# Performance work log

Hardware: AMD Instinct MI355X
Metric: run time of the kernel (lower is better)

## Reference

```python
import jax, jax.numpy as jnp
import numpy as np

N_INST = 50000
D_IN, D_HID, D_ATT = 1024, 512, 256  # size_dict['small']
N_ENS = 4
N_CLS = 2
CB_SIZE = 256
BETA = 0.25
TOP_K = 1


def setup_inputs() -> dict:
    key = jax.random.key(0)
    ks = jax.random.split(key, 9)
    h = jax.random.normal(ks[0], (N_INST, D_IN), dtype=jnp.float32)
    fc_W = jax.random.normal(ks[1], (D_IN, D_HID), dtype=jnp.float32) * (1.0 / np.sqrt(D_IN))
    fc_b = jnp.zeros((D_HID,), dtype=jnp.float32)
    Ua = jax.random.normal(ks[2], (N_ENS, D_HID, D_ATT), dtype=jnp.float32) * (1.0 / np.sqrt(D_HID))
    Ub = jax.random.normal(ks[3], (N_ENS, D_HID, D_ATT), dtype=jnp.float32) * (1.0 / np.sqrt(D_HID))
    Uc = jax.random.normal(ks[4], (N_ENS, D_ATT, 1), dtype=jnp.float32) * (1.0 / np.sqrt(D_ATT))
    cls_W = jax.random.normal(ks[5], (D_HID, N_CLS), dtype=jnp.float32) * (1.0 / np.sqrt(D_HID))
    cls_b = jnp.zeros((N_CLS,), dtype=jnp.float32)
    codebook = jax.random.normal(ks[6], (CB_SIZE, D_HID), dtype=jnp.float32)
    return {"h": h, "fc_W": fc_W, "fc_b": fc_b, "Ua": Ua, "Ub": Ub,
            "Uc": Uc, "cls_W": cls_W, "cls_b": cls_b, "codebook": codebook}


def _vector_quantization(M, codebook):
    # NOTE: original code uses +2*matmul (sign bug in torch source); kept faithful.
    dist = (jnp.sum(M * M, axis=1, keepdims=True)
            + jnp.sum(codebook * codebook, axis=1)
            + 2.0 * (M @ codebook.T))                      # [1, CB]
    inds = jnp.argmin(dist, axis=1)                        # [1]
    one_hot = jax.nn.one_hot(inds, CB_SIZE, dtype=M.dtype)  # [1, CB]
    q = one_hot @ codebook                                  # [1, D_HID]
    commitment = jnp.mean((jax.lax.stop_gradient(q) - M) ** 2)
    embedding = jnp.mean((q - jax.lax.stop_gradient(M)) ** 2)
    vq_loss = commitment * BETA + embedding
    q_st = M + jax.lax.stop_gradient(q - M)  # straight-through (unused downstream)
    return vq_loss, q_st


def reference(h, fc_W, fc_b, Ua, Ub, Uc, cls_W, cls_b, codebook):
    # fc + ReLU: [n, D_HID]
    x = jax.nn.relu(h @ fc_W + fc_b)
    # gated batch-ensemble attention (ensemble dim n=4 broadcast)
    xe = jnp.broadcast_to(x[None], (N_ENS, x.shape[0], D_HID))
    a = jnp.tanh(jnp.einsum('ndk,nkl->ndl', xe, Ua))         # [4, n, D_ATT]
    b = jax.nn.sigmoid(jnp.einsum('ndk,nkl->ndl', xe, Ub))   # [4, n, D_ATT]
    A = jnp.einsum('ndk,nkl->ndl', a * b, Uc).sum(0)          # [n, 1]
    A = jax.nn.sigmoid(A.T)                                   # [1, n]
    M = (A @ x) / jnp.sum(A)                                  # [1, D_HID]
    vq_loss, _M_code = _vector_quantization(M, codebook)
    logits = M @ cls_W + cls_b                                # [1, N_CLS]
    y_probs = jax.nn.softmax(logits, axis=1)
    _, top_idx = jax.lax.top_k(y_probs[:, 1], TOP_K)          # [1]
    top_instance = logits[top_idx]                            # [1, N_CLS]
    Y_hat = jnp.argmax(top_instance, axis=1)[:, None]         # [1, 1] int
    Y_prob = jax.nn.softmax(top_instance, axis=1)
    return (top_instance, Y_prob, Y_hat, vq_loss, y_probs, A)
```

## Files before the change

kernel.cpp:

```cpp
#include <hip/hip_runtime.h>
#include <hip/hip_bf16.h>
#include <math.h>

typedef __bf16 bf16_t;
typedef __bf16 bf16x8 __attribute__((ext_vector_type(8)));
typedef float  f32x4  __attribute__((ext_vector_type(4)));

#define MINST 50000

typedef const __attribute__((address_space(1))) void* gas1_t;
typedef __attribute__((address_space(3))) void* las3_t;
__device__ __forceinline__ void gload16(const void* g, const void* l){
  __builtin_amdgcn_global_load_lds((gas1_t)g, (las3_t)l, 16, 0, 0);
}

__device__ __forceinline__ float fast_sigmoid(float x){
  return __fdividef(1.f, 1.f + __expf(-x));
}
__device__ __forceinline__ float fast_tanh(float x){
  float e = __expf(2.f*x);
  return 1.f - __fdividef(2.f, e + 1.f);
}

__global__ void prep_wt(const float* __restrict__ W, bf16_t* __restrict__ WT){
  int idx = blockIdx.x*256 + threadIdx.x;
  if (idx >= 512*1024) return;
  int n = idx >> 10, k = idx & 1023;
  WT[idx] = (bf16_t)W[k*512 + n];
}

__global__ void prep_uab(const float* __restrict__ Ua, const float* __restrict__ Ub,
                         bf16_t* __restrict__ UabT){
  int idx = blockIdx.x*256 + threadIdx.x;
  if (idx >= 2048*512) return;
  int c = idx >> 9, k = idx & 511;
  int s = c & 1, t = c >> 1;
  int n = t >> 8, l = t & 255;
  const float* src = s ? Ub : Ua;
  UabT[idx] = (bf16_t)src[(n*512 + k)*256 + l];
}

__global__ void zero_ws_k(float* __restrict__ Alogit, float* __restrict__ Mbuf){
  int i = blockIdx.x*256 + threadIdx.x;
  if (i < MINST) Alogit[i] = 0.f;
  if (i < 513)   Mbuf[i]  = 0.f;
}

template<int EPI, int K, int NBY>
__global__ __launch_bounds__(256, 2)
void gemm_k(const void* __restrict__ Ap, const bf16_t* __restrict__ Bp, int M,
            const float* __restrict__ bias, bf16_t* __restrict__ Xout,
            const float* __restrict__ Uc, float* __restrict__ Alogit)
{
  __shared__ bf16_t As[(EPI==0?1:2)][128*32] __attribute__((aligned(16)));
  __shared__ bf16_t Bs[2][128*32] __attribute__((aligned(16)));

  const int tid  = threadIdx.x;
  const int lane = tid & 63;
  const int w    = tid >> 6;
  const int wr   = w >> 1;
  const int wc   = w & 1;

  const int nwg = gridDim.x;
  const int q = nwg >> 3, r = nwg & 7;
  const int x = blockIdx.x & 7, pos = blockIdx.x >> 3;
  const int logical = (x < r ? x*(q+1) : r*(q+1) + (x-r)*q) + pos;
  const int m0 = (logical / NBY) * 128;
  const int n0 = (logical % NBY) * 128;

  const f32x4 fzero = {0.f, 0.f, 0.f, 0.f};
  f32x4 acc[4][4];
#pragma unroll
  for (int m = 0; m < 4; ++m)
#pragma unroll
    for (int n = 0; n < 4; ++n) acc[m][n] = fzero;

  const int srow = lane >> 2;
  const int schk = (lane & 3) * 8;
  const bf16_t* bsrc0 = Bp + (size_t)(n0 + w*32 + srow)*K + schk;
  const bf16_t* bsrc1 = bsrc0 + (size_t)16*K;

  auto stageB = [&](int buf, int k0){
    gload16(bsrc0 + k0, &Bs[buf][(w*32     )*32]);
    gload16(bsrc1 + k0, &Bs[buf][(w*32 + 16)*32]);
  };

  const bf16_t* asrc0 = (const bf16_t*)Ap + (size_t)(m0 + w*32 + srow)*K + schk;
  const bf16_t* asrc1 = asrc0 + (size_t)16*K;
  auto stageA1 = [&](int buf, int k0){
    gload16(asrc0 + k0, &As[buf][(w*32     )*32]);
    gload16(asrc1 + k0, &As[buf][(w*32 + 16)*32]);
  };

  const int a_row  = tid >> 1;
  const int a_half = tid & 1;
  f32x4 sAf[4];
  auto loadA0 = [&](int k0){
    const float* A = (const float*)Ap;
    int gr = m0 + a_row;
    if (gr < M) {
      const f32x4* p = (const f32x4*)(A + (size_t)gr*K + k0 + a_half*16);
      sAf[0]=p[0]; sAf[1]=p[1]; sAf[2]=p[2]; sAf[3]=p[3];
    } else {
      sAf[0]=fzero; sAf[1]=fzero; sAf[2]=fzero; sAf[3]=fzero;
    }
  };
  auto writeA0 = [&](){
    bf16x8 lo, hi;
#pragma unroll
    for (int j = 0; j < 4; ++j) {
      lo[j]   = (bf16_t)sAf[0][j];
      lo[4+j] = (bf16_t)sAf[1][j];
      hi[j]   = (bf16_t)sAf[2][j];
      hi[4+j] = (bf16_t)sAf[3][j];
    }
    *(bf16x8*)&As[0][a_row*32 + a_half*16    ] = lo;
    *(bf16x8*)&As[0][a_row*32 + a_half*16 + 8] = hi;
  };

  const int fr = lane & 15;
  const int kh = lane >> 4;
  constexpr int NT = K / 32;

  if constexpr (EPI == 0) {
    loadA0(0);
    stageB(0, 0);
#pragma unroll 4
    for (int kt = 0; kt < NT; ++kt) {
      const int cur = kt & 1;
      __syncthreads();
      writeA0();
      __syncthreads();
      if (kt + 1 < NT) { loadA0((kt+1)*32); stageB(cur^1, (kt+1)*32); }
      bf16x8 a[4], b[4];
#pragma unroll
      for (int m = 0; m < 4; ++m)
        a[m] = *(const bf16x8*)&As[0][(wr*64 + m*16 + fr)*32 + kh*8];
#pragma unroll
      for (int n = 0; n < 4; ++n)
        b[n] = *(const bf16x8*)&Bs[cur][(wc*64 + n*16 + fr)*32 + kh*8];
#pragma unroll
      for (int m = 0; m < 4; ++m)
#pragma unroll
        for (int n = 0; n < 4; ++n)
          acc[m][n] = __builtin_amdgcn_mfma_f32_16x16x32_bf16(a[m], b[n], acc[m][n], 0, 0, 0);
    }
  } else {
    stageA1(0, 0);
    stageB(0, 0);
#pragma unroll 4
    for (int kt = 0; kt < NT; ++kt) {
      const int cur = kt & 1;
      __syncthreads();
      if (kt + 1 < NT) { stageA1(cur^1, (kt+1)*32); stageB(cur^1, (kt+1)*32); }
      bf16x8 a[4], b[4];
#pragma unroll
      for (int m = 0; m < 4; ++m)
        a[m] = *(const bf16x8*)&As[cur][(wr*64 + m*16 + fr)*32 + kh*8];
#pragma unroll
      for (int n = 0; n < 4; ++n)
        b[n] = *(const bf16x8*)&Bs[cur][(wc*64 + n*16 + fr)*32 + kh*8];
#pragma unroll
      for (int m = 0; m < 4; ++m)
#pragma unroll
        for (int n = 0; n < 4; ++n)
          acc[m][n] = __builtin_amdgcn_mfma_f32_16x16x32_bf16(a[m], b[n], acc[m][n], 0, 0, 0);
    }
  }

  const int rg = lane >> 4;
  if constexpr (EPI == 0) {
#pragma unroll
    for (int n = 0; n < 4; ++n) {
      int col = n0 + wc*64 + n*16 + fr;
      float bv = bias[col];
#pragma unroll
      for (int m = 0; m < 4; ++m)
#pragma unroll
        for (int rr = 0; rr < 4; ++rr) {
          int row = m0 + wr*64 + m*16 + rg*4 + rr;
          if (row < M) {
            float v = acc[m][n][rr] + bv;
            Xout[(size_t)row*512 + col] = (bf16_t)(v > 0.f ? v : 0.f);
          }
        }
    }
  } else {
    float gacc[4][4];
#pragma unroll
    for (int m = 0; m < 4; ++m)
#pragma unroll
      for (int rr = 0; rr < 4; ++rr) gacc[m][rr] = 0.f;
    const bool even = (lane & 1) == 0;
#pragma unroll
    for (int n = 0; n < 4; ++n) {
      int col = n0 + wc*64 + n*16 + fr;
      float ucv = Uc[col >> 1];
#pragma unroll
      for (int m = 0; m < 4; ++m)
#pragma unroll
        for (int rr = 0; rr < 4; ++rr) {
          float v = acc[m][n][rr];
          float tv = even ? fast_tanh(v) : fast_sigmoid(v);
          float pv = __shfl_xor(tv, 1);
          gacc[m][rr] += tv * pv * ucv;
        }
    }
#pragma unroll
    for (int m = 0; m < 4; ++m)
#pragma unroll
      for (int rr = 0; rr < 4; ++rr) {
        float s = gacc[m][rr];
        s += __shfl_xor(s, 1);
        s += __shfl_xor(s, 2);
        s += __shfl_xor(s, 4);
        s += __shfl_xor(s, 8);
        if (fr == 0) {
          int row = m0 + wr*64 + m*16 + rg*4 + rr;
          if (row < M) atomicAdd(&Alogit[row], 0.5f * s);
        }
      }
  }
}

__global__ void a_final(const float* __restrict__ Alogit, float* __restrict__ outA,
                        float* __restrict__ sumA){
  int i = blockIdx.x*256 + threadIdx.x;
  float a = 0.f;
  if (i < MINST) { a = fast_sigmoid(Alogit[i]); outA[i] = a; }
  float s = a;
#pragma unroll
  for (int o = 1; o < 64; o <<= 1) s += __shfl_xor(s, o);
  __shared__ float wsum[4];
  int lane = threadIdx.x & 63, w = threadIdx.x >> 6;
  if (lane == 0) wsum[w] = s;
  __syncthreads();
  if (threadIdx.x == 0) atomicAdd(sumA, wsum[0]+wsum[1]+wsum[2]+wsum[3]);
}

__global__ void m_reduce(const bf16_t* __restrict__ Xb, const float* __restrict__ Aout,
                         float* __restrict__ Mbuf){
  int t = threadIdx.x;
  int c0 = (t & 63) * 8;
  float acc[8];
#pragma unroll
  for (int j = 0; j < 8; ++j) acc[j] = 0.f;
  for (int r = blockIdx.x*4 + (t>>6); r < MINST; r += gridDim.x*4) {
    float a = Aout[r];
    bf16x8 xv = *(const bf16x8*)(Xb + (size_t)r*512 + c0);
#pragma unroll
    for (int j = 0; j < 8; ++j) acc[j] += a * (float)xv[j];
  }
#pragma unroll
  for (int j = 0; j < 8; ++j) atomicAdd(&Mbuf[c0 + j], acc[j]);
}

__device__ __forceinline__ float block_sum256(float v, float* red){
  int t = threadIdx.x;
  red[t] = v; __syncthreads();
  for (int s = 128; s > 0; s >>= 1) {
    if (t < s) red[t] += red[t+s];
    __syncthreads();
  }
  float rr = red[0];
  __syncthreads();
  return rr;
}

__global__ __launch_bounds__(256)
void finalize_k(const float* __restrict__ Mbuf, const float* __restrict__ cb,
                const float* __restrict__ clsW, const float* __restrict__ clsb,
                float* __restrict__ dout)
{
  __shared__ float Mn[512];
  __shared__ float red[256];
  __shared__ float dist[256];
  __shared__ int   idxs[256];
  __shared__ int   indS;
  int t = threadIdx.x;
  float sA = Mbuf[512];
  Mn[t]     = Mbuf[t]     / sA;
  Mn[t+256] = Mbuf[t+256] / sA;
  __syncthreads();
  float msq_p = Mn[t]*Mn[t] + Mn[t+256]*Mn[t+256];
  float Msq = block_sum256(msq_p, red);

  const float* cbr = cb + t*512;
  float cs = 0.f, dt = 0.f;
  for (int k = 0; k < 512; k += 4) {
    f32x4 c = *(const f32x4*)(cbr + k);
    cs += c[0]*c[0] + c[1]*c[1] + c[2]*c[2] + c[3]*c[3];
    dt += Mn[k]*c[0] + Mn[k+1]*c[1] + Mn[k+2]*c[2] + Mn[k+3]*c[3];
  }
  dist[t] = Msq + cs + 2.f*dt;
  idxs[t] = t;
  __syncthreads();
  for (int s = 128; s > 0; s >>= 1) {
    if (t < s && dist[t+s] < dist[t]) { dist[t] = dist[t+s]; idxs[t] = idxs[t+s]; }
    __syncthreads();
  }
  if (t == 0) indS = idxs[0];
  __syncthreads();

  const float* qv = cb + (size_t)indS*512;
  float d0 = qv[t]     - Mn[t];
  float d1 = qv[t+256] - Mn[t+256];
  float vqs = block_sum256(d0*d0 + d1*d1, red);
  float vq_loss = 1.25f * (vqs / 512.f);

  float p0 = Mn[t]*clsW[t*2]   + Mn[t+256]*clsW[(t+256)*2];
  float p1 = Mn[t]*clsW[t*2+1] + Mn[t+256]*clsW[(t+256)*2+1];
  float l0 = block_sum256(p0, red);
  float l1 = block_sum256(p1, red);

  if (t == 0) {
    l0 += clsb[0]; l1 += clsb[1];
    float mx = fmaxf(l0, l1);
    float e0 = __expf(l0 - mx), e1 = __expf(l1 - mx);
    float si = e0 + e1;
    float y0 = e0 / si, y1 = e1 / si;
    int yhat = (l1 > l0) ? 1 : 0;
    dout[0] = l0; dout[1] = l1;
    dout[2] = y0; dout[3] = y1;
    dout[4] = (float)yhat;
    dout[5] = vq_loss;
    dout[6] = y0; dout[7] = y1;
  }
}

extern "C" void kernel_launch(void* const* d_in, const int* in_sizes, int n_in,
                              void* d_out, int out_size, void* d_ws, size_t ws_size,
                              hipStream_t stream) {
  const float* h    = (const float*)d_in[0];
  const float* fcW  = (const float*)d_in[1];
  const float* fcb  = (const float*)d_in[2];
  const float* Ua   = (const float*)d_in[3];
  const float* Ub   = (const float*)d_in[4];
  const float* Uc   = (const float*)d_in[5];
  const float* clsW = (const float*)d_in[6];
  const float* clsb = (const float*)d_in[7];
  const float* cbk  = (const float*)d_in[8];
  float* out = (float*)d_out;

  char* ws = (char*)d_ws;
  bf16_t* Xb     = (bf16_t*)ws;
  bf16_t* WT     = (bf16_t*)(ws + 51200000);
  bf16_t* UabT   = (bf16_t*)(ws + 52248576);
  float*  Alogit = (float*)(ws + 54345728);
  float*  Mbuf   = (float*)(ws + 54545728);

  const int M = MINST;

  prep_wt <<<2048, 256, 0, stream>>>(fcW, WT);
  prep_uab<<<4096, 256, 0, stream>>>(Ua, Ub, UabT);
  zero_ws_k<<<196, 256, 0, stream>>>(Alogit, Mbuf);

  gemm_k<0,1024,4><<<1564, 256, 0, stream>>>(h, WT, M, fcb, Xb, nullptr, nullptr);
  gemm_k<1, 512,16><<<6256, 256, 0, stream>>>(Xb, UabT, M, nullptr, nullptr, Uc, Alogit);

  a_final <<<196, 256, 0, stream>>>(Alogit, out + 8, Mbuf + 512);
  m_reduce<<<128, 256, 0, stream>>>(Xb, out + 8, Mbuf);
  finalize_k<<<1, 256, 0, stream>>>(Mbuf, cbk, clsW, clsb, out);
}
```

Measured before the change: 507.1 us.

## Split GEMM kernels, add multi-chunk triple-buffered attention GEMM with swizzled LDS

The templated GEMM is split in two. The fc GEMM now stages B through registers into padded (stride-40) LDS instead of direct global-to-LDS loads, and uses a plain 2D grid without the XCD remap. The attention GEMM now has each workgroup loop over four 128-column chunks, reusing one A row-tile across 512 output columns. It uses a triple-buffered LDS pipeline with explicit vmcnt waits, an XOR swizzle to avoid bank conflicts, and s_setprio around the MFMAs. The goal is fewer redundant Xb reads, fewer atomics and fewer launches, at the cost of longer-running workgroups; m_reduce also gets twice as many blocks.

```diff
diff --git a/kernel.cpp b/kernel.cpp
--- a/kernel.cpp
+++ b/kernel.cpp
@@ -4,6 +4,7 @@
 
 typedef __bf16 bf16_t;
 typedef __bf16 bf16x8 __attribute__((ext_vector_type(8)));
+typedef __bf16 bf16x2 __attribute__((ext_vector_type(2)));
 typedef float  f32x4  __attribute__((ext_vector_type(4)));
 
 #define MINST 50000
@@ -46,27 +47,20 @@
   if (i < 513)   Mbuf[i]  = 0.f;
 }
 
-template<int EPI, int K, int NBY>
 __global__ __launch_bounds__(256, 2)
-void gemm_k(const void* __restrict__ Ap, const bf16_t* __restrict__ Bp, int M,
-            const float* __restrict__ bias, bf16_t* __restrict__ Xout,
-            const float* __restrict__ Uc, float* __restrict__ Alogit)
+void gemm_fc(const float* __restrict__ Ap, const bf16_t* __restrict__ Bp, int M,
+             const float* __restrict__ bias, bf16_t* __restrict__ Xout)
 {
-  __shared__ bf16_t As[(EPI==0?1:2)][128*32] __attribute__((aligned(16)));
-  __shared__ bf16_t Bs[2][128*32] __attribute__((aligned(16)));
-
+  constexpr int K = 1024;
+  __shared__ bf16_t As[128*40] __attribute__((aligned(16)));
+  __shared__ bf16_t Bs[128*40] __attribute__((aligned(16)));
   const int tid  = threadIdx.x;
   const int lane = tid & 63;
-  const int w    = tid >> 6;
-  const int wr   = w >> 1;
-  const int wc   = w & 1;
-
-  const int nwg = gridDim.x;
-  const int q = nwg >> 3, r = nwg & 7;
-  const int x = blockIdx.x & 7, pos = blockIdx.x >> 3;
-  const int logical = (x < r ? x*(q+1) : r*(q+1) + (x-r)*q) + pos;
-  const int m0 = (logical / NBY) * 128;
-  const int n0 = (logical % NBY) * 128;
+  const int wid  = tid >> 6;
+  const int wr   = wid >> 1;
+  const int wc   = wid & 1;
+  const int m0   = blockIdx.x * 128;
+  const int n0   = blockIdx.y * 128;
 
   const f32x4 fzero = {0.f, 0.f, 0.f, 0.f};
   f32x4 acc[4][4];
@@ -75,37 +69,29 @@
 #pragma unroll
     for (int n = 0; n < 4; ++n) acc[m][n] = fzero;
 
-  const int srow = lane >> 2;
-  const int schk = (lane & 3) * 8;
-  const bf16_t* bsrc0 = Bp + (size_t)(n0 + w*32 + srow)*K + schk;
-  const bf16_t* bsrc1 = bsrc0 + (size_t)16*K;
-
-  auto stageB = [&](int buf, int k0){
-    gload16(bsrc0 + k0, &Bs[buf][(w*32     )*32]);
-    gload16(bsrc1 + k0, &Bs[buf][(w*32 + 16)*32]);
-  };
-
-  const bf16_t* asrc0 = (const bf16_t*)Ap + (size_t)(m0 + w*32 + srow)*K + schk;
-  const bf16_t* asrc1 = asrc0 + (size_t)16*K;
-  auto stageA1 = [&](int buf, int k0){
-    gload16(asrc0 + k0, &As[buf][(w*32     )*32]);
-    gload16(asrc1 + k0, &As[buf][(w*32 + 16)*32]);
-  };
-
+  const int q_row  = tid >> 2;
+  const int q_c    = tid & 3;
   const int a_row  = tid >> 1;
   const int a_half = tid & 1;
-  f32x4 sAf[4];
-  auto loadA0 = [&](int k0){
-    const float* A = (const float*)Ap;
+
+  bf16x8 sB0, sB1;
+  f32x4  sAf[4];
+
+  auto loadTiles = [&](int k0){
+    sB0 = *(const bf16x8*)(Bp + (size_t)(n0 + q_row     )*K + k0 + q_c*8);
+    sB1 = *(const bf16x8*)(Bp + (size_t)(n0 + q_row + 64)*K + k0 + q_c*8);
     int gr = m0 + a_row;
     if (gr < M) {
-      const f32x4* p = (const f32x4*)(A + (size_t)gr*K + k0 + a_half*16);
+      const f32x4* p = (const f32x4*)(Ap + (size_t)gr*K + k0 + a_half*16);
       sAf[0]=p[0]; sAf[1]=p[1]; sAf[2]=p[2]; sAf[3]=p[3];
     } else {
       sAf[0]=fzero; sAf[1]=fzero; sAf[2]=fzero; sAf[3]=fzero;
     }
   };
-  auto writeA0 = [&](){
+
+  auto storeTiles = [&](){
+    *(bf16x8*)&Bs[(q_row     )*40 + q_c*8] = sB0;
+    *(bf16x8*)&Bs[(q_row + 64)*40 + q_c*8] = sB1;
     bf16x8 lo, hi;
 #pragma unroll
     for (int j = 0; j < 4; ++j) {
@@ -114,113 +100,168 @@
       hi[j]   = (bf16_t)sAf[2][j];
       hi[4+j] = (bf16_t)sAf[3][j];
     }
-    *(bf16x8*)&As[0][a_row*32 + a_half*16    ] = lo;
-    *(bf16x8*)&As[0][a_row*32 + a_half*16 + 8] = hi;
+    *(bf16x8*)&As[a_row*40 + a_half*16    ] = lo;
+    *(bf16x8*)&As[a_row*40 + a_half*16 + 8] = hi;
   };
 
+  loadTiles(0);
   const int fr = lane & 15;
   const int kh = lane >> 4;
   constexpr int NT = K / 32;
-
-  if constexpr (EPI == 0) {
-    loadA0(0);
-    stageB(0, 0);
-#pragma unroll 4
-    for (int kt = 0; kt < NT; ++kt) {
-      const int cur = kt & 1;
-      __syncthreads();
-      writeA0();
-      __syncthreads();
-      if (kt + 1 < NT) { loadA0((kt+1)*32); stageB(cur^1, (kt+1)*32); }
-      bf16x8 a[4], b[4];
-#pragma unroll
-      for (int m = 0; m < 4; ++m)
-        a[m] = *(const bf16x8*)&As[0][(wr*64 + m*16 + fr)*32 + kh*8];
+  for (int kt = 0; kt < NT; ++kt) {
+    __syncthreads();
+    storeTiles();
+    __syncthreads();
+    if (kt + 1 < NT) loadTiles((kt+1)*32);
+    bf16x8 a[4], b[4];
+#pragma unroll
+    for (int m = 0; m < 4; ++m)
+      a[m] = *(const bf16x8*)&As[(wr*64 + m*16 + fr)*40 + kh*8];
+#pragma unroll
+    for (int n = 0; n < 4; ++n)
+      b[n] = *(const bf16x8*)&Bs[(wc*64 + n*16 + fr)*40 + kh*8];
+#pragma unroll
+    for (int m = 0; m < 4; ++m)
 #pragma unroll
       for (int n = 0; n < 4; ++n)
-        b[n] = *(const bf16x8*)&Bs[cur][(wc*64 + n*16 + fr)*32 + kh*8];
-#pragma unroll
-      for (int m = 0; m < 4; ++m)
-#pragma unroll
-        for (int n = 0; n < 4; ++n)
-          acc[m][n] = __builtin_amdgcn_mfma_f32_16x16x32_bf16(a[m], b[n], acc[m][n], 0, 0, 0);
-    }
-  } else {
-    stageA1(0, 0);
-    stageB(0, 0);
-#pragma unroll 4
-    for (int kt = 0; kt < NT; ++kt) {
-      const int cur = kt & 1;
-      __syncthreads();
-      if (kt + 1 < NT) { stageA1(cur^1, (kt+1)*32); stageB(cur^1, (kt+1)*32); }
-      bf16x8 a[4], b[4];
-#pragma unroll
-      for (int m = 0; m < 4; ++m)
-        a[m] = *(const bf16x8*)&As[cur][(wr*64 + m*16 + fr)*32 + kh*8];
-#pragma unroll
-      for (int n = 0; n < 4; ++n)
-        b[n] = *(const bf16x8*)&Bs[cur][(wc*64 + n*16 + fr)*32 + kh*8];
-#pragma unroll
-      for (int m = 0; m < 4; ++m)
-#pragma unroll
-        for (int n = 0; n < 4; ++n)
-          acc[m][n] = __builtin_amdgcn_mfma_f32_16x16x32_bf16(a[m], b[n], acc[m][n], 0, 0, 0);
-    }
+        acc[m][n] = __builtin_amdgcn_mfma_f32_16x16x32_bf16(a[m], b[n], acc[m][n], 0, 0, 0);
   }
 
   const int rg = lane >> 4;
-  if constexpr (EPI == 0) {
-#pragma unroll
-    for (int n = 0; n < 4; ++n) {
-      int col = n0 + wc*64 + n*16 + fr;
-      float bv = bias[col];
-#pragma unroll
-      for (int m = 0; m < 4; ++m)
-#pragma unroll
-        for (int rr = 0; rr < 4; ++rr) {
-          int row = m0 + wr*64 + m*16 + rg*4 + rr;
-          if (row < M) {
-            float v = acc[m][n][rr] + bv;
-            Xout[(size_t)row*512 + col] = (bf16_t)(v > 0.f ? v : 0.f);
-          }
-        }
-    }
-  } else {
-    float gacc[4][4];
+#pragma unroll
+  for (int n = 0; n < 4; ++n) {
+    int col = n0 + wc*64 + n*16 + fr;
+    float bv = bias[col];
 #pragma unroll
     for (int m = 0; m < 4; ++m)
 #pragma unroll
-      for (int rr = 0; rr < 4; ++rr) gacc[m][rr] = 0.f;
-    const bool even = (lane & 1) == 0;
-#pragma unroll
-    for (int n = 0; n < 4; ++n) {
-      int col = n0 + wc*64 + n*16 + fr;
-      float ucv = Uc[col >> 1];
-#pragma unroll
-      for (int m = 0; m < 4; ++m)
-#pragma unroll
-        for (int rr = 0; rr < 4; ++rr) {
-          float v = acc[m][n][rr];
-          float tv = even ? fast_tanh(v) : fast_sigmoid(v);
-          float pv = __shfl_xor(tv, 1);
-          gacc[m][rr] += tv * pv * ucv;
-        }
-    }
-#pragma unroll
-    for (int m = 0; m < 4; ++m)
-#pragma unroll
       for (int rr = 0; rr < 4; ++rr) {
-        float s = gacc[m][rr];
-        s += __shfl_xor(s, 1);
-        s += __shfl_xor(s, 2);
-        s += __shfl_xor(s, 4);
-        s += __shfl_xor(s, 8);
-        if (fr == 0) {
-          int row = m0 + wr*64 + m*16 + rg*4 + rr;
-          if (row < M) atomicAdd(&Alogit[row], 0.5f * s);
+        int row = m0 + wr*64 + m*16 + rg*4 + rr;
+        if (row < M) {
+          float v = acc[m][n][rr] + bv;
+          Xout[(size_t)row*512 + col] = (bf16_t)(v > 0.f ? v : 0.f);
         }
       }
   }
+}
+
+__global__ __launch_bounds__(256)
+void gemm_att(const bf16_t* __restrict__ Xb, const bf16_t* __restrict__ Bp, int M,
+              const float* __restrict__ Uc, float* __restrict__ Alogit)
+{
+  constexpr int K = 512, NCH = 4, NTC = 16, TOT = NCH*NTC;
+  __shared__ bf16_t As[3][128*32] __attribute__((aligned(16)));
+  __shared__ bf16_t Bs[3][128*32] __attribute__((aligned(16)));
+
+  const int tid  = threadIdx.x;
+  const int lane = tid & 63;
+  const int w    = tid >> 6;
+  const int wr   = w >> 1;
+  const int wc   = w & 1;
+
+  const int nwg = gridDim.x;
+  const int q = nwg >> 3, r = nwg & 7;
+  const int x = blockIdx.x & 7, pos = blockIdx.x >> 3;
+  const int logical = (x < r ? x*(q+1) : r*(q+1) + (x-r)*q) + pos;
+  const int m0 = (logical >> 2) * 128;
+  const int nb = (logical & 3) * 512;
+
+  const f32x4 fzero = {0.f, 0.f, 0.f, 0.f};
+  f32x4 acc[4][4];
+  float gacc[4][4];
+#pragma unroll
+  for (int m = 0; m < 4; ++m)
+#pragma unroll
+    for (int n = 0; n < 4; ++n){ acc[m][n] = fzero; gacc[m][n] = 0.f; }
+
+  const int sr  = lane >> 2;
+  const int scc = (lane & 3) ^ ((lane >> 3) & 3);
+  const bf16_t* aS0 = Xb + (size_t)(m0 + w*32 +      sr)*K + scc*8;
+  const bf16_t* aS1 = Xb + (size_t)(m0 + w*32 + 16 + sr)*K + scc*8;
+  const bf16_t* bS0 = Bp + (size_t)(nb + w*32 +      sr)*K + scc*8;
+  const bf16_t* bS1 = Bp + (size_t)(nb + w*32 + 16 + sr)*K + scc*8;
+
+  auto stage = [&](int it2, int buf){
+    const int c2  = it2 >> 4;
+    const int kt2 = it2 & 15;
+    const size_t boff = (size_t)c2*(128*K) + kt2*32;
+    gload16(aS0 + kt2*32, &As[buf][(w*32     )*32]);
+    gload16(aS1 + kt2*32, &As[buf][(w*32 + 16)*32]);
+    gload16(bS0 + boff,   &Bs[buf][(w*32     )*32]);
+    gload16(bS1 + boff,   &Bs[buf][(w*32 + 16)*32]);
+  };
+
+  const int fr = lane & 15;
+  const int kh = lane >> 4;
+  const int ca = (kh ^ ((fr >> 1) & 3)) * 8;
+  const bool even = (lane & 1) == 0;
+
+  stage(0, 0);
+  stage(1, 1);
+  int cur = 0, sb = 2;
+  for (int it = 0; it < TOT; ++it){
+    if (it + 1 < TOT) asm volatile("s_waitcnt vmcnt(4)" ::: "memory");
+    else              asm volatile("s_waitcnt vmcnt(0)" ::: "memory");
+    __builtin_amdgcn_s_barrier();
+    if (it + 2 < TOT) stage(it+2, sb);
+
+    bf16x8 a[4], b[4];
+#pragma unroll
+    for (int m = 0; m < 4; ++m)
+      a[m] = *(const bf16x8*)&As[cur][(wr*64 + m*16 + fr)*32 + ca];
+#pragma unroll
+    for (int n = 0; n < 4; ++n)
+      b[n] = *(const bf16x8*)&Bs[cur][(wc*64 + n*16 + fr)*32 + ca];
+
+    __builtin_amdgcn_s_setprio(1);
+#pragma unroll
+    for (int m = 0; m < 4; ++m)
+#pragma unroll
+      for (int n = 0; n < 4; ++n)
+        acc[m][n] = __builtin_amdgcn_mfma_f32_16x16x32_bf16(a[m], b[n], acc[m][n], 0, 0, 0);
+    __builtin_amdgcn_s_setprio(0);
+
+    if ((it & 15) == 15){
+      const int c = it >> 4;
+#pragma unroll
+      for (int n = 0; n < 4; ++n){
+        int col = nb + c*128 + wc*64 + n*16 + fr;
+        float ucv = Uc[col >> 1];
+#pragma unroll
+        for (int m = 0; m < 4; ++m)
+#pragma unroll
+          for (int rr = 0; rr < 4; ++rr){
+            float v = acc[m][n][rr];
+            float tv = even ? fast_tanh(v) : fast_sigmoid(v);
+            float pv = __shfl_xor(tv, 1);
+            gacc[m][rr] += tv * pv * ucv;
+          }
+      }
+#pragma unroll
+      for (int m = 0; m < 4; ++m)
+#pragma unroll
+        for (int n = 0; n < 4; ++n) acc[m][n] = fzero;
+    }
+
+    cur = (cur == 2) ? 0 : cur + 1;
+    sb  = (sb  == 2) ? 0 : sb  + 1;
+  }
+
+  const int rg = lane >> 4;
+#pragma unroll
+  for (int m = 0; m < 4; ++m)
+#pragma unroll
+    for (int rr = 0; rr < 4; ++rr){
+      float s = gacc[m][rr];
+      s += __shfl_xor(s, 1);
+      s += __shfl_xor(s, 2);
+      s += __shfl_xor(s, 4);
+      s += __shfl_xor(s, 8);
+      if (fr == 0){
+        int row = m0 + wr*64 + m*16 + rg*4 + rr;
+        if (row < M) atomicAdd(&Alogit[row], 0.5f * s);
+      }
+    }
 }
 
 __global__ void a_final(const float* __restrict__ Alogit, float* __restrict__ outA,
@@ -355,10 +396,10 @@
   prep_uab<<<4096, 256, 0, stream>>>(Ua, Ub, UabT);
   zero_ws_k<<<196, 256, 0, stream>>>(Alogit, Mbuf);
 
-  gemm_k<0,1024,4><<<1564, 256, 0, stream>>>(h, WT, M, fcb, Xb, nullptr, nullptr);
-  gemm_k<1, 512,16><<<6256, 256, 0, stream>>>(Xb, UabT, M, nullptr, nullptr, Uc, Alogit);
+  gemm_fc<<<dim3(391, 4), 256, 0, stream>>>(h, WT, M, fcb, Xb);
+  gemm_att<<<1564, 256, 0, stream>>>(Xb, UabT, M, Uc, Alogit);
 
   a_final <<<196, 256, 0, stream>>>(Alogit, out + 8, Mbuf + 512);
-  m_reduce<<<128, 256, 0, stream>>>(Xb, out + 8, Mbuf);
+  m_reduce<<<256, 256, 0, stream>>>(Xb, out + 8, Mbuf);
   finalize_k<<<1, 256, 0, stream>>>(Mbuf, cbk, clsW, clsb, out);
 }
```

New measurement: 717.3 us. 1.41x slower.
